# Kernel tuning notes

Hardware: AMD Instinct MI355X
Metric: run time of the kernel (lower is better)

Reference implementation:

```python
import jax, jax.numpy as jnp
import numpy as np

N = 8388608

def setup_inputs() -> dict:
    key = jax.random.key(0)
    k1, k2 = jax.random.split(key)
    preds = jax.random.normal(k1, (N, 5), dtype=jnp.float32)
    target = jax.random.normal(k2, (N, 3), dtype=jnp.float32)
    return {"preds": preds, "target": target}

def reference(preds, target):
    # main MSE over the first 3 quantile columns: [N, 3]
    main_mse = (preds[:, :3] - target[:, :3]) ** 2

    p2 = preds[:, 2]
    p3 = preds[:, 3]
    t2 = target[:, 2]

    # lower-range loss, vectorized form of the per-row if/elif/else: [N]
    lower = jnp.where(
        p3 > p2,
        jnp.float32(1000.0),
        jnp.where(p3 > t2 * 0.95, jnp.float32(0.0), (p3 - t2 * 0.95) ** 2),
    )

    # NOTE: the original code assigns upper_range_loss = torch.Tensor(lowe_range_loss),
    # i.e. the upper range loss is (buggily) a copy of the lower range loss.
    # We replicate that behavior faithfully.
    upper = lower

    # concatenate all loss elements (3N + N + N) and reduce with mean
    loss = jnp.concatenate([main_mse.ravel(), lower, upper])
    return jnp.mean(loss)
```

## Files before the change

### kernel.cpp

```cpp
#include <hip/hip_runtime.h>


#define NROWS 8388608
#define ROWS_PER_CHUNK 1024
#define NCHUNKS (NROWS / ROWS_PER_CHUNK)
#define PCHUNK (ROWS_PER_CHUNK * 5)
#define TCHUNK (ROWS_PER_CHUNK * 3)
#define GRID 2048
#define CHUNKS_PER_BLOCK (NCHUNKS / GRID)

typedef float v4f __attribute__((ext_vector_type(4)));

__global__ void __launch_bounds__(256) qloss_partial(
    const float* __restrict__ preds,
    const float* __restrict__ target,
    double* __restrict__ ws)
{
    __shared__ float sp[PCHUNK];
    __shared__ float st[TCHUNK];

    const int t = threadIdx.x;
    double acc = 0.0;

    v4f rp[5], rt[3];
    {
        const v4f* gp = (const v4f*)(preds + (size_t)blockIdx.x * PCHUNK);
        const v4f* gt = (const v4f*)(target + (size_t)blockIdx.x * TCHUNK);
        #pragma unroll
        for (int k = 0; k < 5; ++k) rp[k] = __builtin_nontemporal_load(gp + t + k * 256);
        #pragma unroll
        for (int k = 0; k < 3; ++k) rt[k] = __builtin_nontemporal_load(gt + t + k * 256);
    }

    #pragma unroll
    for (int i = 0; i < CHUNKS_PER_BLOCK; ++i) {
        #pragma unroll
        for (int k = 0; k < 5; ++k) ((v4f*)sp)[t + k * 256] = rp[k];
        #pragma unroll
        for (int k = 0; k < 3; ++k) ((v4f*)st)[t + k * 256] = rt[k];
        __syncthreads();

        if (i + 1 < CHUNKS_PER_BLOCK) {
            const int nc = blockIdx.x + (i + 1) * GRID;
            const v4f* gp = (const v4f*)(preds + (size_t)nc * PCHUNK);
            const v4f* gt = (const v4f*)(target + (size_t)nc * TCHUNK);
            #pragma unroll
            for (int k = 0; k < 5; ++k) rp[k] = __builtin_nontemporal_load(gp + t + k * 256);
            #pragma unroll
            for (int k = 0; k < 3; ++k) rt[k] = __builtin_nontemporal_load(gt + t + k * 256);
        }

        float sum = 0.0f;
        #pragma unroll
        for (int rr = 0; rr < 4; ++rr) {
            const int r = t + rr * 256;
            const float p0 = sp[5*r + 0];
            const float p1 = sp[5*r + 1];
            const float p2 = sp[5*r + 2];
            const float p3 = sp[5*r + 3];
            const float t0 = st[3*r + 0];
            const float t1 = st[3*r + 1];
            const float t2 = st[3*r + 2];

            const float a0 = p0 - t0;
            const float a1 = p1 - t1;
            const float a2 = p2 - t2;
            const float m  = a0*a0 + a1*a1 + a2*a2;

            const float q = t2 * 0.95f;
            const float d = p3 - q;
            const float lower = (p3 > p2) ? 1000.0f : ((p3 > q) ? 0.0f : d * d);

            sum += m + 2.0f * lower;
        }
        acc += (double)sum;
        __syncthreads();
    }

    #pragma unroll
    for (int off = 32; off > 0; off >>= 1)
        acc += __shfl_down(acc, off, 64);

    __shared__ double red[4];
    const int lane = t & 63;
    const int wave = t >> 6;
    if (lane == 0) red[wave] = acc;
    __syncthreads();

    if (t == 0)
        atomicAdd(ws, red[0] + red[1] + red[2] + red[3]);

}

__global__ void qloss_final(const double* __restrict__ ws, float* __restrict__ out)
{
    *out = (float)(*ws / (5.0 * (double)NROWS));
}

extern "C" void kernel_launch(void* const* d_in, const int* in_sizes, int n_in,
                              void* d_out, int out_size, void* d_ws, size_t ws_size,
                              hipStream_t stream)
{
    const float* preds  = (const float*)d_in[0];
    const float* target = (const float*)d_in[1];
    float* out  = (float*)d_out;
    double* ws  = (double*)d_ws;

    hipMemsetAsync(ws, 0, sizeof(double), stream);

    qloss_partial<<<GRID, 256, 0, stream>>>(preds, target, ws);
    qloss_final<<<1, 1, 0, stream>>>(ws, out);
}
```

Before: 280.1 us.

## Launch one block per chunk and replace atomic sum with two-stage reduction

The persistent 2048-block loop with register prefetch is replaced by 8192 blocks, each handling one 1024-row chunk. Each block writes its partial sum to its own workspace slot, and a 256-thread final kernel reduces those slots, which removes the atomic add and the memset launch. Loads also switch from nontemporal to ordinary. The aim is more parallelism and less launch and atomic overhead, at the cost of losing the cross-iteration prefetch overlap and paying more per-block startup work.

```diff
diff --git a/kernel.cpp b/kernel.cpp
--- a/kernel.cpp
+++ b/kernel.cpp
@@ -6,8 +6,6 @@
 #define NCHUNKS (NROWS / ROWS_PER_CHUNK)
 #define PCHUNK (ROWS_PER_CHUNK * 5)
 #define TCHUNK (ROWS_PER_CHUNK * 3)
-#define GRID 2048
-#define CHUNKS_PER_BLOCK (NCHUNKS / GRID)
 
 typedef float v4f __attribute__((ext_vector_type(4)));
 
@@ -20,62 +18,46 @@
     __shared__ float st[TCHUNK];
 
     const int t = threadIdx.x;
-    double acc = 0.0;
+    const int c = blockIdx.x;
 
+    const v4f* gp = (const v4f*)(preds + (size_t)c * PCHUNK);
+    const v4f* gt = (const v4f*)(target + (size_t)c * TCHUNK);
     v4f rp[5], rt[3];
-    {
-        const v4f* gp = (const v4f*)(preds + (size_t)blockIdx.x * PCHUNK);
-        const v4f* gt = (const v4f*)(target + (size_t)blockIdx.x * TCHUNK);
-        #pragma unroll
-        for (int k = 0; k < 5; ++k) rp[k] = __builtin_nontemporal_load(gp + t + k * 256);
-        #pragma unroll
-        for (int k = 0; k < 3; ++k) rt[k] = __builtin_nontemporal_load(gt + t + k * 256);
-    }
+    #pragma unroll
+    for (int k = 0; k < 5; ++k) rp[k] = gp[t + k * 256];
+    #pragma unroll
+    for (int k = 0; k < 3; ++k) rt[k] = gt[t + k * 256];
 
     #pragma unroll
-    for (int i = 0; i < CHUNKS_PER_BLOCK; ++i) {
-        #pragma unroll
-        for (int k = 0; k < 5; ++k) ((v4f*)sp)[t + k * 256] = rp[k];
-        #pragma unroll
-        for (int k = 0; k < 3; ++k) ((v4f*)st)[t + k * 256] = rt[k];
-        __syncthreads();
+    for (int k = 0; k < 5; ++k) ((v4f*)sp)[t + k * 256] = rp[k];
+    #pragma unroll
+    for (int k = 0; k < 3; ++k) ((v4f*)st)[t + k * 256] = rt[k];
+    __syncthreads();
 
-        if (i + 1 < CHUNKS_PER_BLOCK) {
-            const int nc = blockIdx.x + (i + 1) * GRID;
-            const v4f* gp = (const v4f*)(preds + (size_t)nc * PCHUNK);
-            const v4f* gt = (const v4f*)(target + (size_t)nc * TCHUNK);
-            #pragma unroll
-            for (int k = 0; k < 5; ++k) rp[k] = __builtin_nontemporal_load(gp + t + k * 256);
-            #pragma unroll
-            for (int k = 0; k < 3; ++k) rt[k] = __builtin_nontemporal_load(gt + t + k * 256);
-        }
+    float sum = 0.0f;
+    #pragma unroll
+    for (int rr = 0; rr < 4; ++rr) {
+        const int r = t + rr * 256;
+        const float p0 = sp[5*r + 0];
+        const float p1 = sp[5*r + 1];
+        const float p2 = sp[5*r + 2];
+        const float p3 = sp[5*r + 3];
+        const float t0 = st[3*r + 0];
+        const float t1 = st[3*r + 1];
+        const float t2 = st[3*r + 2];
 
-        float sum = 0.0f;
-        #pragma unroll
-        for (int rr = 0; rr < 4; ++rr) {
-            const int r = t + rr * 256;
-            const float p0 = sp[5*r + 0];
-            const float p1 = sp[5*r + 1];
-            const float p2 = sp[5*r + 2];
-            const float p3 = sp[5*r + 3];
-            const float t0 = st[3*r + 0];
-            const float t1 = st[3*r + 1];
-            const float t2 = st[3*r + 2];
+        const float a0 = p0 - t0;
+        const float a1 = p1 - t1;
+        const float a2 = p2 - t2;
+        const float m  = a0*a0 + a1*a1 + a2*a2;
 
-            const float a0 = p0 - t0;
-            const float a1 = p1 - t1;
-            const float a2 = p2 - t2;
-            const float m  = a0*a0 + a1*a1 + a2*a2;
+        const float q = t2 * 0.95f;
+        const float d = p3 - q;
+        const float lower = (p3 > p2) ? 1000.0f : ((p3 > q) ? 0.0f : d * d);
 
-            const float q = t2 * 0.95f;
-            const float d = p3 - q;
-            const float lower = (p3 > p2) ? 1000.0f : ((p3 > q) ? 0.0f : d * d);
-
-            sum += m + 2.0f * lower;
-        }
-        acc += (double)sum;
-        __syncthreads();
+        sum += m + 2.0f * lower;
     }
+    double acc = (double)sum;
 
     #pragma unroll
     for (int off = 32; off > 0; off >>= 1)
@@ -88,13 +70,30 @@
     __syncthreads();
 
     if (t == 0)
-        atomicAdd(ws, red[0] + red[1] + red[2] + red[3]);
-
+        ws[c] = red[0] + red[1] + red[2] + red[3];
 }
 
-__global__ void qloss_final(const double* __restrict__ ws, float* __restrict__ out)
+__global__ void __launch_bounds__(256) qloss_final(
+    const double* __restrict__ ws, float* __restrict__ out)
 {
-    *out = (float)(*ws / (5.0 * (double)NROWS));
+    const int t = threadIdx.x;
+    double acc = 0.0;
+    #pragma unroll
+    for (int i = 0; i < NCHUNKS / 256; ++i)
+        acc += ws[t + i * 256];
+
+    #pragma unroll
+    for (int off = 32; off > 0; off >>= 1)
+        acc += __shfl_down(acc, off, 64);
+
+    __shared__ double red[4];
+    const int lane = t & 63;
+    const int wave = t >> 6;
+    if (lane == 0) red[wave] = acc;
+    __syncthreads();
+
+    if (t == 0)
+        *out = (float)((red[0] + red[1] + red[2] + red[3]) / (5.0 * (double)NROWS));
 }
 
 extern "C" void kernel_launch(void* const* d_in, const int* in_sizes, int n_in,
@@ -106,8 +105,6 @@
     float* out  = (float*)d_out;
     double* ws  = (double*)d_ws;
 
-    hipMemsetAsync(ws, 0, sizeof(double), stream);
-
-    qloss_partial<<<GRID, 256, 0, stream>>>(preds, target, ws);
-    qloss_final<<<1, 1, 0, stream>>>(ws, out);
+    qloss_partial<<<NCHUNKS, 256, 0, stream>>>(preds, target, ws);
+    qloss_final<<<1, 256, 0, stream>>>(ws, out);
 }
```

Measured after the change: 293.1 us. +4.7%, slower.
